# Optimization experiments

Measured on AMD Instinct MI355X. Metric: run time of the kernel, lower is better.

Reference implementation:

```python
import jax, jax.numpy as jnp
import numpy as np

N_NODES = 50000
N_EDGES = 1600000
FEAT = 64


def setup_inputs() -> dict:
    key = jax.random.key(0)
    k1, k2, k3, k4 = jax.random.split(key, 4)
    nodes = jax.random.normal(k1, (N_NODES, FEAT), dtype=jnp.float32)
    neighbor_feats = jax.random.normal(k2, (N_EDGES, FEAT), dtype=jnp.float32)
    attention = jax.random.uniform(k3, (N_EDGES,), dtype=jnp.float32)
    bias = jnp.zeros((FEAT,), dtype=jnp.float32)  # init_params zero-inits bias
    segment_ids = jnp.sort(jax.random.randint(k4, (N_EDGES,), 0, N_NODES, dtype=jnp.int32))
    return {"nodes": nodes, "neighbor_feats": neighbor_feats, "attention": attention,
            "bias": bias, "segment_ids": segment_ids}


def reference(nodes, neighbor_feats, attention, bias, segment_ids):
    # Per node i: sum_j attn[i,j] * neigh[i,j]  (ragged loop in torch ->
    # fused weighted segment-sum over the flattened edge list), then + bias.
    weighted = neighbor_feats * attention[:, None]          # [E, F]
    out = jax.ops.segment_sum(weighted, segment_ids, num_segments=N_NODES)  # [N, F]
    return out + bias
```

## Files before the change

kernel.cpp:

```cpp
#include <hip/hip_runtime.h>


#define FEAT 64

__global__ __launch_bounds__(256) void boundaries_kernel(
    const int* __restrict__ seg,
    int* __restrict__ offs,
    int n_edges, int n_nodes)
{
    const int e = blockIdx.x * blockDim.x + threadIdx.x;
    if (e >= n_edges) return;
    const int s = seg[e];
    if (e == 0) {
        for (int n = 0; n <= s; ++n) offs[n] = 0;
    } else {
        const int sp = seg[e - 1];
        if (sp != s)
            for (int n = sp + 1; n <= s; ++n) offs[n] = e;
    }
    if (e == n_edges - 1) {
        for (int n = s + 1; n <= n_nodes; ++n) offs[n] = n_edges;
    }
}

__global__ __launch_bounds__(256) void segsum_kernel(
    const float* __restrict__ neigh,
    const float* __restrict__ att,
    const float* __restrict__ bias,
    const int*   __restrict__ offs,
    float* __restrict__ out,
    int n_nodes)
{
    const int wave_id = (blockIdx.x * blockDim.x + threadIdx.x) >> 6;
    const int lane    = threadIdx.x & 63;
    if (wave_id >= n_nodes) return;
    const int node = wave_id;

    const int start = offs[node];
    const int end   = offs[node + 1];

    const int rowgrp = lane >> 4;
    const int colgrp = lane & 15;

    float4 acc0 = make_float4(0.f, 0.f, 0.f, 0.f);
    float4 acc1 = make_float4(0.f, 0.f, 0.f, 0.f);

    int e = start;
    for (; e + 8 <= end; e += 8) {
        const int r0 = e + rowgrp;
        const int r1 = e + 4 + rowgrp;
        const float  a0 = att[r0];
        const float4 v0 = *(const float4*)(neigh + (size_t)r0 * FEAT + colgrp * 4);
        const float  a1 = att[r1];
        const float4 v1 = *(const float4*)(neigh + (size_t)r1 * FEAT + colgrp * 4);
        acc0.x = fmaf(a0, v0.x, acc0.x);
        acc0.y = fmaf(a0, v0.y, acc0.y);
        acc0.z = fmaf(a0, v0.z, acc0.z);
        acc0.w = fmaf(a0, v0.w, acc0.w);
        acc1.x = fmaf(a1, v1.x, acc1.x);
        acc1.y = fmaf(a1, v1.y, acc1.y);
        acc1.z = fmaf(a1, v1.z, acc1.z);
        acc1.w = fmaf(a1, v1.w, acc1.w);
    }
    if (e + 4 <= end) {
        const int r = e + rowgrp;
        const float  a = att[r];
        const float4 v = *(const float4*)(neigh + (size_t)r * FEAT + colgrp * 4);
        acc0.x = fmaf(a, v.x, acc0.x);
        acc0.y = fmaf(a, v.y, acc0.y);
        acc0.z = fmaf(a, v.z, acc0.z);
        acc0.w = fmaf(a, v.w, acc0.w);
        e += 4;
    }
    if (e + rowgrp < end) {
        const int r = e + rowgrp;
        const float  a = att[r];
        const float4 v = *(const float4*)(neigh + (size_t)r * FEAT + colgrp * 4);
        acc1.x = fmaf(a, v.x, acc1.x);
        acc1.y = fmaf(a, v.y, acc1.y);
        acc1.z = fmaf(a, v.z, acc1.z);
        acc1.w = fmaf(a, v.w, acc1.w);
    }

    float4 acc;
    acc.x = acc0.x + acc1.x;
    acc.y = acc0.y + acc1.y;
    acc.z = acc0.z + acc1.z;
    acc.w = acc0.w + acc1.w;

    #pragma unroll
    for (int off = 32; off >= 16; off >>= 1) {
        acc.x += __shfl_down(acc.x, off);
        acc.y += __shfl_down(acc.y, off);
        acc.z += __shfl_down(acc.z, off);
        acc.w += __shfl_down(acc.w, off);
    }

    if (rowgrp == 0) {
        const float4 b = *(const float4*)(bias + colgrp * 4);
        float4 o;
        o.x = acc.x + b.x;
        o.y = acc.y + b.y;
        o.z = acc.z + b.z;
        o.w = acc.w + b.w;
        *(float4*)(out + (size_t)node * FEAT + colgrp * 4) = o;
    }
}

extern "C" void kernel_launch(void* const* d_in, const int* in_sizes, int n_in,
                              void* d_out, int out_size, void* d_ws, size_t ws_size,
                              hipStream_t stream) {
    const float* neigh = (const float*)d_in[1];
    const float* att   = (const float*)d_in[2];
    const float* bias  = (const float*)d_in[3];
    const int*   seg   = (const int*)d_in[4];
    float* out = (float*)d_out;

    const int n_edges = in_sizes[2];
    const int n_nodes = out_size / FEAT;

    int* offs = (int*)d_ws;

    boundaries_kernel<<<(n_edges + 255) / 256, 256, 0, stream>>>(
        seg, offs, n_edges, n_nodes);

    const int waves_per_block = 256 / 64;
    const int blocks = (n_nodes + waves_per_block - 1) / waves_per_block;
    segsum_kernel<<<blocks, 256, 0, stream>>>(neigh, att, bias, offs, out,
                                              n_nodes);
}
```

Before: 546.7 us.

## Assign four nodes per wave with a grid-stride persistent loop

Each wave now handles four nodes at once, one per 16-lane quarter, and no longer splits one node's edges across the four row groups. That removes the cross-lane shuffle reduction. The grid is fixed at 2048 blocks that loop over node quads, and the bias is loaded once per thread. The trade-offs are possible divergence when the four nodes have different edge counts, and a loss of contiguous 4-row reads within a node. There is also no bounds check for node >= n_nodes when n_nodes is not a multiple of 4, which is safe here because 50000 divides by 4.

```diff
diff --git a/kernel.cpp b/kernel.cpp
--- a/kernel.cpp
+++ b/kernel.cpp
@@ -23,7 +23,11 @@
     }
 }
 
-__global__ __launch_bounds__(256) void segsum_kernel(
+#define BLOCKS 2048
+#define THREADS 256
+#define TOTAL_WAVES (BLOCKS * (THREADS / 64))
+
+__global__ __launch_bounds__(THREADS) void segsum_kernel(
     const float* __restrict__ neigh,
     const float* __restrict__ att,
     const float* __restrict__ bias,
@@ -31,79 +35,52 @@
     float* __restrict__ out,
     int n_nodes)
 {
-    const int wave_id = (blockIdx.x * blockDim.x + threadIdx.x) >> 6;
+    const int wave_id = blockIdx.x * (THREADS / 64) + (threadIdx.x >> 6);
     const int lane    = threadIdx.x & 63;
-    if (wave_id >= n_nodes) return;
-    const int node = wave_id;
+    const int q       = lane >> 4;
+    const int col     = (lane & 15) * 4;
 
-    const int start = offs[node];
-    const int end   = offs[node + 1];
+    const float4 b = *(const float4*)(bias + col);
+    const int n_quads = (n_nodes + 3) >> 2;
 
-    const int rowgrp = lane >> 4;
-    const int colgrp = lane & 15;
+    for (int quad = wave_id; quad < n_quads; quad += TOTAL_WAVES) {
+        const int node = quad * 4 + q;
+        const int start = offs[node];
+        const int end   = offs[node + 1];
 
-    float4 acc0 = make_float4(0.f, 0.f, 0.f, 0.f);
-    float4 acc1 = make_float4(0.f, 0.f, 0.f, 0.f);
+        float4 acc0 = make_float4(0.f, 0.f, 0.f, 0.f);
+        float4 acc1 = make_float4(0.f, 0.f, 0.f, 0.f);
 
-    int e = start;
-    for (; e + 8 <= end; e += 8) {
-        const int r0 = e + rowgrp;
-        const int r1 = e + 4 + rowgrp;
-        const float  a0 = att[r0];
-        const float4 v0 = *(const float4*)(neigh + (size_t)r0 * FEAT + colgrp * 4);
-        const float  a1 = att[r1];
-        const float4 v1 = *(const float4*)(neigh + (size_t)r1 * FEAT + colgrp * 4);
-        acc0.x = fmaf(a0, v0.x, acc0.x);
-        acc0.y = fmaf(a0, v0.y, acc0.y);
-        acc0.z = fmaf(a0, v0.z, acc0.z);
-        acc0.w = fmaf(a0, v0.w, acc0.w);
-        acc1.x = fmaf(a1, v1.x, acc1.x);
-        acc1.y = fmaf(a1, v1.y, acc1.y);
-        acc1.z = fmaf(a1, v1.z, acc1.z);
-        acc1.w = fmaf(a1, v1.w, acc1.w);
-    }
-    if (e + 4 <= end) {
-        const int r = e + rowgrp;
-        const float  a = att[r];
-        const float4 v = *(const float4*)(neigh + (size_t)r * FEAT + colgrp * 4);
-        acc0.x = fmaf(a, v.x, acc0.x);
-        acc0.y = fmaf(a, v.y, acc0.y);
-        acc0.z = fmaf(a, v.z, acc0.z);
-        acc0.w = fmaf(a, v.w, acc0.w);
-        e += 4;
-    }
-    if (e + rowgrp < end) {
-        const int r = e + rowgrp;
-        const float  a = att[r];
-        const float4 v = *(const float4*)(neigh + (size_t)r * FEAT + colgrp * 4);
-        acc1.x = fmaf(a, v.x, acc1.x);
-        acc1.y = fmaf(a, v.y, acc1.y);
-        acc1.z = fmaf(a, v.z, acc1.z);
-        acc1.w = fmaf(a, v.w, acc1.w);
-    }
+        int r = start;
+        for (; r + 2 <= end; r += 2) {
+            const float  a0 = att[r];
+            const float4 v0 = *(const float4*)(neigh + (size_t)r * FEAT + col);
+            const float  a1 = att[r + 1];
+            const float4 v1 = *(const float4*)(neigh + (size_t)(r + 1) * FEAT + col);
+            acc0.x = fmaf(a0, v0.x, acc0.x);
+            acc0.y = fmaf(a0, v0.y, acc0.y);
+            acc0.z = fmaf(a0, v0.z, acc0.z);
+            acc0.w = fmaf(a0, v0.w, acc0.w);
+            acc1.x = fmaf(a1, v1.x, acc1.x);
+            acc1.y = fmaf(a1, v1.y, acc1.y);
+            acc1.z = fmaf(a1, v1.z, acc1.z);
+            acc1.w = fmaf(a1, v1.w, acc1.w);
+        }
+        if (r < end) {
+            const float  a = att[r];
+            const float4 v = *(const float4*)(neigh + (size_t)r * FEAT + col);
+            acc0.x = fmaf(a, v.x, acc0.x);
+            acc0.y = fmaf(a, v.y, acc0.y);
+            acc0.z = fmaf(a, v.z, acc0.z);
+            acc0.w = fmaf(a, v.w, acc0.w);
+        }
 
-    float4 acc;
-    acc.x = acc0.x + acc1.x;
-    acc.y = acc0.y + acc1.y;
-    acc.z = acc0.z + acc1.z;
-    acc.w = acc0.w + acc1.w;
-
-    #pragma unroll
-    for (int off = 32; off >= 16; off >>= 1) {
-        acc.x += __shfl_down(acc.x, off);
-        acc.y += __shfl_down(acc.y, off);
-        acc.z += __shfl_down(acc.z, off);
-        acc.w += __shfl_down(acc.w, off);
-    }
-
-    if (rowgrp == 0) {
-        const float4 b = *(const float4*)(bias + colgrp * 4);
         float4 o;
-        o.x = acc.x + b.x;
-        o.y = acc.y + b.y;
-        o.z = acc.z + b.z;
-        o.w = acc.w + b.w;
-        *(float4*)(out + (size_t)node * FEAT + colgrp * 4) = o;
+        o.x = acc0.x + acc1.x + b.x;
+        o.y = acc0.y + acc1.y + b.y;
+        o.z = acc0.z + acc1.z + b.z;
+        o.w = acc0.w + acc1.w + b.w;
+        *(float4*)(out + (size_t)node * FEAT + col) = o;
     }
 }
 
@@ -124,8 +101,6 @@
     boundaries_kernel<<<(n_edges + 255) / 256, 256, 0, stream>>>(
         seg, offs, n_edges, n_nodes);
 
-    const int waves_per_block = 256 / 64;
-    const int blocks = (n_nodes + waves_per_block - 1) / waves_per_block;
-    segsum_kernel<<<blocks, 256, 0, stream>>>(neigh, att, bias, offs, out,
-                                              n_nodes);
+    segsum_kernel<<<BLOCKS, THREADS, 0, stream>>>(neigh, att, bias, offs, out,
+                                                  n_nodes);
 }
```

Result: no change. 557.4 us (+2.0%).
